# Optimization experiments

Measured on AMD Instinct MI355X. Metric: run time of the kernel, lower is better.

## Reference

```python
import jax, jax.numpy as jnp
import numpy as np
from jax import lax

B, C, H, W = 32, 684, 16, 64
HID, A, CK, K = 256, 512, 512, 11


def setup_inputs() -> dict:
    key = jax.random.key(0)
    ks = jax.random.split(key, 12)
    s = 0.02
    return {
        "cnn_features": jax.random.normal(ks[0], (B, C, H, W), jnp.float32),
        "hidden": jax.random.normal(ks[1], (B, HID), jnp.float32),
        "alpha_sum": jax.random.uniform(ks[2], (B, 1, H, W), jnp.float32),
        "image_mask": jnp.ones((B, 1, H, W), jnp.float32),
        # hidden_weight: Linear(HID -> A)
        "Wh": jax.random.normal(ks[3], (A, HID), jnp.float32) * s,
        "bh": jnp.zeros((A,), jnp.float32),
        # encoder_feature_conv: Conv2d(C -> A, 1x1) == pointwise linear
        "Wec": jax.random.normal(ks[4], (A, C), jnp.float32) * s,
        "bec": jnp.zeros((A,), jnp.float32),
        # attention_conv: Conv2d(1 -> CK, 11x11, pad 5, no bias)
        "Wac": jax.random.normal(ks[5], (CK, 1, K, K), jnp.float32) * s,
        # attention_weight: Linear(CK -> A, no bias)
        "Waw": jax.random.normal(ks[6], (A, CK), jnp.float32) * s,
        # alpha_convert: Linear(A -> 1)
        "Wv": jax.random.normal(ks[7], (1, A), jnp.float32) * s,
        "bv": jnp.zeros((1,), jnp.float32),
    }


def reference(cnn_features, hidden, alpha_sum, image_mask,
              Wh, bh, Wec, bec, Wac, Waw, Wv, bv):
    # query = hidden_weight(hidden): [B, A]
    query = hidden @ Wh.T + bh
    # attention_conv(alpha_sum): [B, CK, H, W]
    ast = lax.conv_general_dilated(
        alpha_sum, Wac, window_strides=(1, 1),
        padding=[(K // 2, K // 2), (K // 2, K // 2)],
        dimension_numbers=("NCHW", "OIHW", "NCHW"))
    # attention_weight on permuted conv output: [B, H, W, A]
    coverage_alpha = jnp.einsum("bkhw,ak->bhwa", ast, Waw)
    # encoder_feature_conv (1x1 conv == pointwise linear): [B, H, W, A]
    cnn_trans = jnp.einsum("bchw,ac->bhwa", cnn_features, Wec) + bec
    # additive attention score
    alpha_score = jnp.tanh(query[:, None, None, :] + coverage_alpha + cnn_trans)
    # alpha_convert -> scalar energy per position: [B, H, W]
    energy = jnp.einsum("bhwa,a->bhw", alpha_score, Wv[0]) + bv[0]
    energy = energy - energy.max()  # global max-subtract as in original
    energy_exp = jnp.exp(energy) * image_mask[:, 0]
    denom = energy_exp.sum(axis=(-1, -2))[:, None, None] + 1e-10
    alpha = energy_exp / denom  # [B, H, W]
    alpha_sum_new = alpha[:, None, :, :] + alpha_sum  # [B, 1, H, W]
    # context: weighted spatial sum over features -> [B, C]
    context_vector = jnp.einsum("bhw,bchw->bc", alpha, cnn_features)
    return (context_vector, alpha, alpha_sum_new)
```

## Files before the change

kernel.cpp:

```cpp
#include <hip/hip_runtime.h>
#include <math.h>

#define Bn   32
#define Cn   684
#define Hn   16
#define Wn   64
#define HWn  1024
#define HIDn 256
#define An   512
#define KKn  121
#define CREAL 805
#define CPAD 832
#define NSTEP 26
#define NBLK 256

#define OUT_ALPHA 21888
#define OUT_ASUM  (21888 + 32768)

typedef short short8 __attribute__((ext_vector_type(8)));
typedef float floatx4 __attribute__((ext_vector_type(4)));

__device__ __forceinline__ unsigned short f2bf(float f) {
    union { float f; unsigned int i; } v; v.f = f;
    unsigned int i = v.i;
    return (unsigned short)((i + 0x7fffu + ((i >> 16) & 1u)) >> 16);
}
__device__ __forceinline__ unsigned int pack2bf(float v0, float v1) {
    unsigned int u0 = __float_as_uint(v0), u1 = __float_as_uint(v1);
    u0 = (u0 + 0x7fffu + ((u0 >> 16) & 1u)) >> 16;
    u1 = (u1 + 0x7fffu + ((u1 >> 16) & 1u)) & 0xffff0000u;
    return u0 | u1;
}
__device__ __forceinline__ void async_lds16(void* lds, const void* g) {
    __builtin_amdgcn_global_load_lds(
        (const __attribute__((address_space(1))) unsigned int*)g,
        (__attribute__((address_space(3))) unsigned int*)lds, 16, 0, 0);
}

__global__ __launch_bounds__(256) void k_prep(
    const float* __restrict__ hidden,
    const float* __restrict__ Wh,
    const float* __restrict__ bh,
    const float* __restrict__ bec,
    const float* __restrict__ Wec,
    const float* __restrict__ Wac,
    const float* __restrict__ Waw,
    float* __restrict__ query,
    unsigned short* __restrict__ VTbf)
{
    __shared__ float sbuf[512];
    const int blk = blockIdx.x, t = threadIdx.x;
    if (blk < 512) {
        const int a = blk;
        sbuf[t]       = Waw[(size_t)a * 512 + t];
        sbuf[t + 256] = Waw[(size_t)a * 512 + t + 256];
        __syncthreads();
        for (int cp = t; cp < Cn; cp += 256)
            VTbf[(size_t)a * CPAD + cp] = f2bf(Wec[(size_t)a * Cn + cp]);
        if (t < KKn) {
            float s = 0.f;
            #pragma unroll 8
            for (int k = 0; k < 512; ++k)
                s = fmaf(sbuf[k], Wac[k * KKn + t], s);
            VTbf[(size_t)a * CPAD + Cn + t] = f2bf(s);
        }
        for (int cp = CREAL + t; cp < CPAD; cp += 256)
            VTbf[(size_t)a * CPAD + cp] = 0;
    } else {
        const int b = blk - 512;
        sbuf[t] = (t < HIDn) ? hidden[b * HIDn + t] : 0.f;
        __syncthreads();
        for (int a = t; a < An; a += 256) {
            const float4* wp = (const float4*)(Wh + (size_t)a * HIDn);
            float s = bh[a] + bec[a];
            #pragma unroll 8
            for (int i = 0; i < HIDn / 4; ++i) {
                float4 w = wp[i];
                s = fmaf(sbuf[4 * i],     w.x, s);
                s = fmaf(sbuf[4 * i + 1], w.y, s);
                s = fmaf(sbuf[4 * i + 2], w.z, s);
                s = fmaf(sbuf[4 * i + 3], w.w, s);
            }
            query[b * An + a] = s;
        }
    }
}

__device__ __forceinline__ float fetchU(const float* __restrict__ X,
                                        const float* plane,
                                        int m, int row) {
    if (row < Cn)   return X[(size_t)row * HWn + m];
    if (row < CREAL) {
        int ij = row - Cn; int di = ij / 11, dj = ij - di * 11;
        return plane[di * 74 + m + dj];
    }
    return 0.f;
}

__global__ __launch_bounds__(256, 3) void k_energy(
    const float* __restrict__ X,
    const float* __restrict__ asum,
    const float* __restrict__ Wv,
    const float* __restrict__ query,
    const unsigned short* __restrict__ VTbf,
    float* __restrict__ energy)
{
    __shared__ unsigned short As[2 * 64 * 40];
    __shared__ unsigned short Bs[2 * 256 * 32];
    __shared__ float plane[11 * 74 + 2];
    __shared__ float qs[NBLK];
    __shared__ float wvs[NBLK];

    const int t = threadIdx.x;
    const int nh = blockIdx.x, hh = blockIdx.y, b = blockIdx.z;
    const int w = t >> 6, lane = t & 63;
    const int q = lane >> 4, r = lane & 15;
    const int nbase = nh * NBLK;
    const int mA = t & 63;
    const int koA = t >> 6;

    const float* Xb = X + (size_t)b * Cn * HWn + hh * Wn;

    for (int i = t; i < 11 * 74; i += 256) {
        int di = i / 74, cc = i - di * 74;
        int h2 = hh + di - 5, w2 = cc - 5;
        float v = 0.f;
        if (h2 >= 0 && h2 < Hn && w2 >= 0 && w2 < Wn)
            v = asum[b * HWn + h2 * Wn + w2];
        plane[i] = v;
    }
    qs[t]  = query[b * An + nbase + t];
    wvs[t] = Wv[nbase + t];
    {
        const float* xp = Xb + (size_t)(koA * 8) * HWn + mA;
        unsigned int pk[4];
        #pragma unroll
        for (int jj = 0; jj < 4; ++jj)
            pk[jj] = pack2bf(xp[(size_t)(2 * jj) * HWn], xp[(size_t)(2 * jj + 1) * HWn]);
        *(uint4*)&As[mA * 40 + koA * 8] = make_uint4(pk[0], pk[1], pk[2], pk[3]);
    }
    #pragma unroll
    for (int ii = 0; ii < 4; ++ii) {
        int n0 = w * 64 + ii * 16;
        int row = nbase + n0 + (lane >> 2);
        int gc = (lane & 3) ^ ((lane >> 2) & 3);
        async_lds16(&Bs[n0 * 32], VTbf + (size_t)row * CPAD + gc * 8);
    }
    __syncthreads();

    floatx4 acc[4][4];
    #pragma unroll
    for (int mf = 0; mf < 4; ++mf)
        #pragma unroll
        for (int nf = 0; nf < 4; ++nf)
            acc[mf][nf] = (floatx4){0.f, 0.f, 0.f, 0.f};

    for (int ch = 0; ch < NSTEP; ++ch) {
        const int cur = ch & 1;
        const unsigned short* Ab = As + cur * (64 * 40);
        const unsigned short* Bb = Bs + cur * (256 * 32);

        short8 af[4], bfr[4];
        #pragma unroll
        for (int mf = 0; mf < 4; ++mf)
            af[mf] = *(const short8*)&Ab[(mf * 16 + r) * 40 + q * 8];
        #pragma unroll
        for (int nf = 0; nf < 4; ++nf)
            bfr[nf] = *(const short8*)&Bb[(w * 64 + nf * 16 + r) * 32 + (q ^ (r & 3)) * 8];

        if (ch < NSTEP - 1) {
            const int c1 = (ch + 1) * 32;
            unsigned short* Bn_ = Bs + (cur ^ 1) * (256 * 32);
            #pragma unroll
            for (int ii = 0; ii < 4; ++ii) {
                int n0 = w * 64 + ii * 16;
                int row = nbase + n0 + (lane >> 2);
                int gc = (lane & 3) ^ ((lane >> 2) & 3);
                async_lds16(&Bn_[n0 * 32], VTbf + (size_t)row * CPAD + c1 + gc * 8);
            }
            unsigned int pk[4];
            if (c1 + 31 < Cn) {
                const float* xp = Xb + (size_t)(c1 + koA * 8) * HWn + mA;
                #pragma unroll
                for (int jj = 0; jj < 4; ++jj)
                    pk[jj] = pack2bf(xp[(size_t)(2 * jj) * HWn],
                                     xp[(size_t)(2 * jj + 1) * HWn]);
            } else {
                float v[8];
                #pragma unroll
                for (int jj = 0; jj < 8; ++jj)
                    v[jj] = fetchU(Xb, plane, mA, c1 + koA * 8 + jj);
                #pragma unroll
                for (int jj = 0; jj < 4; ++jj)
                    pk[jj] = pack2bf(v[2 * jj], v[2 * jj + 1]);
            }
            *(uint4*)&As[(cur ^ 1) * (64 * 40) + mA * 40 + koA * 8] =
                make_uint4(pk[0], pk[1], pk[2], pk[3]);
        }

        #pragma unroll
        for (int mf = 0; mf < 4; ++mf)
            #pragma unroll
            for (int nf = 0; nf < 4; ++nf)
                acc[mf][nf] = __builtin_amdgcn_mfma_f32_16x16x32_bf16(
                    af[mf], bfr[nf], acc[mf][nf], 0, 0, 0);

        __syncthreads();
    }

    float ep[16];
    #pragma unroll
    for (int i = 0; i < 16; ++i) ep[i] = 0.f;
    #pragma unroll
    for (int nf = 0; nf < 4; ++nf) {
        int nl = w * 64 + nf * 16 + r;
        float qv = qs[nl], wv = wvs[nl];
        #pragma unroll
        for (int mf = 0; mf < 4; ++mf)
            #pragma unroll
            for (int rg = 0; rg < 4; ++rg) {
                float x = acc[mf][nf][rg] + qv;
                float e2 = __expf(2.f * x);
                float th = 1.f - 2.f * __builtin_amdgcn_rcpf(e2 + 1.f);
                ep[mf * 4 + rg] += wv * th;
            }
    }
    float* red = (float*)Bs;
    #pragma unroll
    for (int mf = 0; mf < 4; ++mf)
        #pragma unroll
        for (int rg = 0; rg < 4; ++rg)
            red[(mf * 16 + q * 4 + rg) * 65 + w * 16 + r] = ep[mf * 4 + rg];
    __syncthreads();
    if (t < 64) {
        float s = 0.f;
        #pragma unroll 16
        for (int i = 0; i < 64; ++i) s += red[t * 65 + i];
        atomicAdd(&energy[b * HWn + hh * Wn + t], s);
    }
}

__global__ __launch_bounds__(256) void k_ctx(
    const float* __restrict__ X,
    const float* __restrict__ energy,
    const float* __restrict__ mask,
    const float* __restrict__ asum,
    float* __restrict__ out)
{
    __shared__ float al[1024];
    __shared__ float rsm[8];
    const int bx = blockIdx.x, b = blockIdx.y;
    const int t = threadIdx.x, lane = t & 63, wid = t >> 6;

    float e[4], ex[4];
    #pragma unroll
    for (int i = 0; i < 4; ++i) e[i] = energy[b * HWn + i * 256 + t];
    float m = fmaxf(fmaxf(e[0], e[1]), fmaxf(e[2], e[3]));
    for (int off = 32; off >= 1; off >>= 1) m = fmaxf(m, __shfl_down(m, off, 64));
    if (lane == 0) rsm[wid] = m;
    __syncthreads();
    if (t == 0)
        rsm[4] = fmaxf(fmaxf(rsm[0], rsm[1]), fmaxf(rsm[2], rsm[3]));
    __syncthreads();
    const float M = rsm[4];
    float s = 0.f;
    #pragma unroll
    for (int i = 0; i < 4; ++i) {
        ex[i] = expf(e[i] - M) * mask[b * HWn + i * 256 + t];
        s += ex[i];
    }
    for (int off = 32; off >= 1; off >>= 1) s += __shfl_down(s, off, 64);
    __syncthreads();
    if (lane == 0) rsm[wid] = s;
    __syncthreads();
    if (t == 0) rsm[5] = rsm[0] + rsm[1] + rsm[2] + rsm[3] + 1e-10f;
    __syncthreads();
    const float denom = rsm[5];
    #pragma unroll
    for (int i = 0; i < 4; ++i) al[i * 256 + t] = ex[i] / denom;
    __syncthreads();

    const int c = bx * 4 + wid;
    const float* xp = X + ((size_t)(b * Cn + c)) * HWn;
    float s2 = 0.f;
    #pragma unroll
    for (int i = 0; i < 4; ++i) {
        int off = i * 256 + lane * 4;
        float4 x = *(const float4*)(xp + off);
        float4 a = *(const float4*)(al + off);
        s2 = fmaf(a.x, x.x, s2);
        s2 = fmaf(a.y, x.y, s2);
        s2 = fmaf(a.z, x.z, s2);
        s2 = fmaf(a.w, x.w, s2);
    }
    for (int off = 32; off >= 1; off >>= 1) s2 += __shfl_down(s2, off, 64);
    if (lane == 0) out[b * Cn + c] = s2;

    if (bx == 0) {
        #pragma unroll
        for (int i = 0; i < 4; ++i) {
            int p = i * 256 + t;
            float a = al[p];
            out[OUT_ALPHA + b * HWn + p] = a;
            out[OUT_ASUM  + b * HWn + p] = a + asum[b * HWn + p];
        }
    }
}

extern "C" void kernel_launch(void* const* d_in, const int* in_sizes, int n_in,
                              void* d_out, int out_size, void* d_ws, size_t ws_size,
                              hipStream_t stream)
{
    const float* X      = (const float*)d_in[0];
    const float* hidden = (const float*)d_in[1];
    const float* asum   = (const float*)d_in[2];
    const float* mask   = (const float*)d_in[3];
    const float* Wh     = (const float*)d_in[4];
    const float* bh     = (const float*)d_in[5];
    const float* Wec    = (const float*)d_in[6];
    const float* bec    = (const float*)d_in[7];
    const float* Wac    = (const float*)d_in[8];
    const float* Waw    = (const float*)d_in[9];
    const float* Wv     = (const float*)d_in[10];
    (void)in_sizes; (void)n_in; (void)out_size; (void)ws_size;

    float* out = (float*)d_out;
    float* ws = (float*)d_ws;
    float* query  = ws;
    float* energy = ws + 16384;
    unsigned short* VTbf = (unsigned short*)(ws + 16384 + 32768);

    hipMemsetAsync(energy, 0, HWn * Bn * sizeof(float), stream);
    k_prep   <<<dim3(544),      dim3(256), 0, stream>>>(hidden, Wh, bh, bec,
                                                        Wec, Wac, Waw, query, VTbf);
    k_energy <<<dim3(2, 16, 32), dim3(256), 0, stream>>>(X, asum, Wv, query, VTbf, energy);
    k_ctx    <<<dim3(171, 32),  dim3(256), 0, stream>>>(X, energy, mask, asum, out);
}
```

Measured before the change: 253.9 us.

## Overlap X loads with MFMA, refine LDS swizzle, split softmax from context kernel

In the energy GEMM, the next chunk's fp32 feature loads are issued before the MFMAs, and the bf16 pack and LDS store happen after them, so global load latency is hidden behind compute. The B-tile XOR swizzle gains an extra term to cut LDS bank conflicts. Softmax normalization moves into its own small kernel that writes alpha once, so the 171x32 context blocks no longer each redo the max/sum reductions. The cost is one more kernel launch and more live registers in the GEMM loop.

```diff
diff --git a/kernel.cpp b/kernel.cpp
--- a/kernel.cpp
+++ b/kernel.cpp
@@ -105,8 +105,8 @@
     const unsigned short* __restrict__ VTbf,
     float* __restrict__ energy)
 {
-    __shared__ unsigned short As[2 * 64 * 40];
-    __shared__ unsigned short Bs[2 * 256 * 32];
+    __shared__ __align__(16) unsigned short As[2 * 64 * 40];
+    __shared__ __align__(16) unsigned short Bs[2 * 256 * 32];
     __shared__ float plane[11 * 74 + 2];
     __shared__ float qs[NBLK];
     __shared__ float wvs[NBLK];
@@ -121,6 +121,8 @@
 
     const float* Xb = X + (size_t)b * Cn * HWn + hh * Wn;
 
+    const int gcw = (lane & 3) ^ ((lane >> 2) & 3) ^ ((lane >> 4) & 3);
+
     for (int i = t; i < 11 * 74; i += 256) {
         int di = i / 74, cc = i - di * 74;
         int h2 = hh + di - 5, w2 = cc - 5;
@@ -143,8 +145,7 @@
     for (int ii = 0; ii < 4; ++ii) {
         int n0 = w * 64 + ii * 16;
         int row = nbase + n0 + (lane >> 2);
-        int gc = (lane & 3) ^ ((lane >> 2) & 3);
-        async_lds16(&Bs[n0 * 32], VTbf + (size_t)row * CPAD + gc * 8);
+        async_lds16(&Bs[n0 * 32], VTbf + (size_t)row * CPAD + gcw * 8);
     }
     __syncthreads();
 
@@ -166,36 +167,30 @@
             af[mf] = *(const short8*)&Ab[(mf * 16 + r) * 40 + q * 8];
         #pragma unroll
         for (int nf = 0; nf < 4; ++nf)
-            bfr[nf] = *(const short8*)&Bb[(w * 64 + nf * 16 + r) * 32 + (q ^ (r & 3)) * 8];
-
-        if (ch < NSTEP - 1) {
+            bfr[nf] = *(const short8*)&Bb[(w * 64 + nf * 16 + r) * 32 +
+                                          ((q ^ (r & 3) ^ ((r >> 2) & 3)) * 8)];
+
+        const bool stage = (ch < NSTEP - 1);
+        float av[8];
+        if (stage) {
             const int c1 = (ch + 1) * 32;
+            if (c1 + 31 < Cn) {
+                const float* xp = Xb + (size_t)(c1 + koA * 8) * HWn + mA;
+                #pragma unroll
+                for (int jj = 0; jj < 8; ++jj)
+                    av[jj] = xp[(size_t)jj * HWn];
+            } else {
+                #pragma unroll
+                for (int jj = 0; jj < 8; ++jj)
+                    av[jj] = fetchU(Xb, plane, mA, c1 + koA * 8 + jj);
+            }
             unsigned short* Bn_ = Bs + (cur ^ 1) * (256 * 32);
             #pragma unroll
             for (int ii = 0; ii < 4; ++ii) {
                 int n0 = w * 64 + ii * 16;
                 int row = nbase + n0 + (lane >> 2);
-                int gc = (lane & 3) ^ ((lane >> 2) & 3);
-                async_lds16(&Bn_[n0 * 32], VTbf + (size_t)row * CPAD + c1 + gc * 8);
+                async_lds16(&Bn_[n0 * 32], VTbf + (size_t)row * CPAD + c1 + gcw * 8);
             }
-            unsigned int pk[4];
-            if (c1 + 31 < Cn) {
-                const float* xp = Xb + (size_t)(c1 + koA * 8) * HWn + mA;
-                #pragma unroll
-                for (int jj = 0; jj < 4; ++jj)
-                    pk[jj] = pack2bf(xp[(size_t)(2 * jj) * HWn],
-                                     xp[(size_t)(2 * jj + 1) * HWn]);
-            } else {
-                float v[8];
-                #pragma unroll
-                for (int jj = 0; jj < 8; ++jj)
-                    v[jj] = fetchU(Xb, plane, mA, c1 + koA * 8 + jj);
-                #pragma unroll
-                for (int jj = 0; jj < 4; ++jj)
-                    pk[jj] = pack2bf(v[2 * jj], v[2 * jj + 1]);
-            }
-            *(uint4*)&As[(cur ^ 1) * (64 * 40) + mA * 40 + koA * 8] =
-                make_uint4(pk[0], pk[1], pk[2], pk[3]);
         }
 
         #pragma unroll
@@ -204,6 +199,15 @@
             for (int nf = 0; nf < 4; ++nf)
                 acc[mf][nf] = __builtin_amdgcn_mfma_f32_16x16x32_bf16(
                     af[mf], bfr[nf], acc[mf][nf], 0, 0, 0);
+
+        if (stage) {
+            unsigned int pk[4];
+            #pragma unroll
+            for (int jj = 0; jj < 4; ++jj)
+                pk[jj] = pack2bf(av[2 * jj], av[2 * jj + 1]);
+            *(uint4*)&As[(cur ^ 1) * (64 * 40) + mA * 40 + koA * 8] =
+                make_uint4(pk[0], pk[1], pk[2], pk[3]);
+        }
 
         __syncthreads();
     }
@@ -240,16 +244,14 @@
     }
 }
 
-__global__ __launch_bounds__(256) void k_ctx(
-    const float* __restrict__ X,
-    const float* __restrict__ energy,
+__global__ __launch_bounds__(256) void k_softmax(
     const float* __restrict__ mask,
     const float* __restrict__ asum,
+    float* __restrict__ energy,
     float* __restrict__ out)
 {
-    __shared__ float al[1024];
     __shared__ float rsm[8];
-    const int bx = blockIdx.x, b = blockIdx.y;
+    const int b = blockIdx.x;
     const int t = threadIdx.x, lane = t & 63, wid = t >> 6;
 
     float e[4], ex[4];
@@ -277,7 +279,26 @@
     __syncthreads();
     const float denom = rsm[5];
     #pragma unroll
-    for (int i = 0; i < 4; ++i) al[i * 256 + t] = ex[i] / denom;
+    for (int i = 0; i < 4; ++i) {
+        int p = i * 256 + t;
+        float a = ex[i] / denom;
+        energy[b * HWn + p] = a;
+        out[OUT_ALPHA + b * HWn + p] = a;
+        out[OUT_ASUM  + b * HWn + p] = a + asum[b * HWn + p];
+    }
+}
+
+__global__ __launch_bounds__(256) void k_ctx(
+    const float* __restrict__ X,
+    const float* __restrict__ alpha,
+    float* __restrict__ out)
+{
+    __shared__ float al[1024];
+    const int bx = blockIdx.x, b = blockIdx.y;
+    const int t = threadIdx.x, lane = t & 63, wid = t >> 6;
+
+    #pragma unroll
+    for (int i = 0; i < 4; ++i) al[i * 256 + t] = alpha[b * HWn + i * 256 + t];
     __syncthreads();
 
     const int c = bx * 4 + wid;
@@ -295,16 +316,6 @@
     }
     for (int off = 32; off >= 1; off >>= 1) s2 += __shfl_down(s2, off, 64);
     if (lane == 0) out[b * Cn + c] = s2;
-
-    if (bx == 0) {
-        #pragma unroll
-        for (int i = 0; i < 4; ++i) {
-            int p = i * 256 + t;
-            float a = al[p];
-            out[OUT_ALPHA + b * HWn + p] = a;
-            out[OUT_ASUM  + b * HWn + p] = a + asum[b * HWn + p];
-        }
-    }
 }
 
 extern "C" void kernel_launch(void* const* d_in, const int* in_sizes, int n_in,
@@ -331,8 +342,9 @@
     unsigned short* VTbf = (unsigned short*)(ws + 16384 + 32768);
 
     hipMemsetAsync(energy, 0, HWn * Bn * sizeof(float), stream);
-    k_prep   <<<dim3(544),      dim3(256), 0, stream>>>(hidden, Wh, bh, bec,
-                                                        Wec, Wac, Waw, query, VTbf);
-    k_energy <<<dim3(2, 16, 32), dim3(256), 0, stream>>>(X, asum, Wv, query, VTbf, energy);
-    k_ctx    <<<dim3(171, 32),  dim3(256), 0, stream>>>(X, energy, mask, asum, out);
-}
+    k_prep    <<<dim3(544),       dim3(256), 0, stream>>>(hidden, Wh, bh, bec,
+                                                          Wec, Wac, Waw, query, VTbf);
+    k_energy  <<<dim3(2, 16, 32), dim3(256), 0, stream>>>(X, asum, Wv, query, VTbf, energy);
+    k_softmax <<<dim3(32),        dim3(256), 0, stream>>>(mask, asum, energy, out);
+    k_ctx     <<<dim3(171, 32),   dim3(256), 0, stream>>>(X, energy, out);
+}
```

Measured after the change: 272.6 us. +7.4%, slower.
